# Optimization experiments

Measured on AMD Instinct MI355X. Metric: run time of the kernel, lower is better.

Reference implementation:

```python
import jax, jax.numpy as jnp
import numpy as np
import math

V, E, H, L, S_MAX = 50257, 1024, 16, 4, 1024
D = E // H
F = 4 * E
B, S = 2, 1024


def _ln(x, w, b, eps=1e-5):
    mu = jnp.mean(x, axis=-1, keepdims=True)
    var = jnp.var(x, axis=-1, keepdims=True)
    return (x - mu) * jax.lax.rsqrt(var + eps) * w + b


def setup_inputs() -> dict:
    key = jax.random.key(0)
    ks = jax.random.split(key, 16)
    std = 0.02
    def nrm(k, shape):
        return jax.random.normal(k, shape, dtype=jnp.float32) * std
    inp = {
        'idx': jax.random.randint(ks[0], (B, S), 0, V),
        'tok_emb': nrm(ks[1], (V, E)),
        'pos_emb': jnp.zeros((S_MAX, E), jnp.float32),
        # per-layer stacked params; Linear weights stored [in, out]
        'ln1_w': jnp.ones((L, E), jnp.float32), 'ln1_b': jnp.zeros((L, E), jnp.float32),
        'Wq': nrm(ks[2], (L, E, E)), 'bq': jnp.zeros((L, E), jnp.float32),
        'Wk': nrm(ks[3], (L, E, E)), 'bk': jnp.zeros((L, E), jnp.float32),
        'Wv': nrm(ks[4], (L, E, E)), 'bv': jnp.zeros((L, E), jnp.float32),
        'Wo': nrm(ks[5], (L, E, E)), 'bo': jnp.zeros((L, E), jnp.float32),
        'ln2_w': jnp.ones((L, E), jnp.float32), 'ln2_b': jnp.zeros((L, E), jnp.float32),
        'W1': nrm(ks[6], (L, E, F)), 'b1': jnp.zeros((L, F), jnp.float32),
        'W2': nrm(ks[7], (L, F, E)), 'b2': jnp.zeros((L, E), jnp.float32),
        'lnf_w': jnp.ones((E,), jnp.float32), 'lnf_b': jnp.zeros((E,), jnp.float32),
        'head_W': nrm(ks[8], (V, E)),  # torch Linear weight [out, in], no bias
    }
    return inp


def _gpt(idx, tok_emb, pos_emb, ln1_w, ln1_b, Wq, bq, Wk, bk, Wv, bv, Wo, bo,
         ln2_w, ln2_b, W1, b1, W2, b2, lnf_w, lnf_b, head_W):
    b, s = idx.shape
    x = tok_emb[idx] + pos_emb[None, :s, :]  # [B,S,E]
    causal = jnp.tril(jnp.ones((s, s), bool))
    scale = 1.0 / math.sqrt(D)
    for l in range(L):
        h = _ln(x, ln1_w[l], ln1_b[l])
        q = (h @ Wq[l] + bq[l]).reshape(b, s, H, D).transpose(0, 2, 1, 3)
        k = (h @ Wk[l] + bk[l]).reshape(b, s, H, D).transpose(0, 2, 1, 3)
        v = (h @ Wv[l] + bv[l]).reshape(b, s, H, D).transpose(0, 2, 1, 3)
        scores = jnp.einsum('bhsd,bhtd->bhst', q, k) * scale
        scores = jnp.where(causal, scores, -jnp.inf)
        attn = jax.nn.softmax(scores, axis=-1)
        y = jnp.einsum('bhst,bhtd->bhsd', attn, v)
        y = y.transpose(0, 2, 1, 3).reshape(b, s, E)
        x = x + y @ Wo[l] + bo[l]
        h2 = _ln(x, ln2_w[l], ln2_b[l])
        x = x + jax.nn.gelu(h2 @ W1[l] + b1[l], approximate=False) @ W2[l] + b2[l]
    x = _ln(x, lnf_w, lnf_b)
    return x @ head_W.T  # logits [B,S,V]


def reference(idx, tok_emb, pos_emb, ln1_w, ln1_b, Wq, bq, Wk, bk, Wv, bv, Wo, bo,
              ln2_w, ln2_b, W1, b1, W2, b2, lnf_w, lnf_b, head_W):
    return _gpt(idx, tok_emb, pos_emb, ln1_w, ln1_b, Wq, bq, Wk, bk, Wv, bv, Wo, bo,
                ln2_w, ln2_b, W1, b1, W2, b2, lnf_w, lnf_b, head_W)
```

## Files before the change

kernel.cpp:

```cpp
#include <hip/hip_runtime.h>
#include <hip/hip_bf16.h>
#include <math.h>

#define E_DIM 1024
#define H_NUM 16
#define D_DIM 64
#define F_DIM 4096
#define L_NUM 4
#define B_NUM 2
#define S_LEN 1024
#define V_DIM 50257
#define M_TOK 2048

typedef __attribute__((ext_vector_type(8))) short s8v;
typedef __attribute__((ext_vector_type(4))) float f4v;

static __device__ __forceinline__ float bf2f(unsigned short u) {
    union { unsigned int i; float f; } c; c.i = ((unsigned int)u) << 16; return c.f;
}
static __device__ __forceinline__ unsigned short f2bf(float f) {
    union { float f; unsigned int i; } c; c.f = f;
    unsigned int r = c.i + 0x7FFFu + ((c.i >> 16) & 1u);
    return (unsigned short)(r >> 16);
}

static __device__ __forceinline__ void gload16(const ushort* g, ushort* l) {
    __builtin_amdgcn_global_load_lds(
        (const __attribute__((address_space(1))) unsigned int*)g,
        (__attribute__((address_space(3))) unsigned int*)l, 16, 0, 0);
}

__global__ void embed_kernel(const int* __restrict__ idx,
                             const float* __restrict__ tok,
                             const float* __restrict__ pos,
                             float* __restrict__ x) {
    int row = blockIdx.x;
    int s = row & (S_LEN - 1);
    int t = idx[row];
    const float* te = tok + (size_t)t * E_DIM;
    const float* pe = pos + (size_t)s * E_DIM;
    float* xr = x + (size_t)row * E_DIM;
    int c = threadIdx.x * 4;
    float4 a = *(const float4*)(te + c);
    float4 p = *(const float4*)(pe + c);
    float4 o; o.x = a.x + p.x; o.y = a.y + p.y; o.z = a.z + p.z; o.w = a.w + p.w;
    *(float4*)(xr + c) = o;
}

__global__ void ln_kernel(const float* __restrict__ x,
                          const float* __restrict__ w,
                          const float* __restrict__ b,
                          ushort* __restrict__ out) {
    int row = blockIdx.x;
    const float* xr = x + (size_t)row * E_DIM;
    int tid = threadIdx.x;
    float4 v = *(const float4*)(xr + tid * 4);
    float s  = v.x + v.y + v.z + v.w;
    float s2 = v.x*v.x + v.y*v.y + v.z*v.z + v.w*v.w;
    #pragma unroll
    for (int m = 32; m >= 1; m >>= 1) {
        s  += __shfl_xor(s,  m, 64);
        s2 += __shfl_xor(s2, m, 64);
    }
    __shared__ float red[8];
    int wid = tid >> 6;
    if ((tid & 63) == 0) { red[wid] = s; red[wid + 4] = s2; }
    __syncthreads();
    s  = red[0] + red[1] + red[2] + red[3];
    s2 = red[4] + red[5] + red[6] + red[7];
    float mu  = s * (1.0f / E_DIM);
    float var = s2 * (1.0f / E_DIM) - mu * mu;
    float rs  = rsqrtf(var + 1e-5f);
    float4 wv = *(const float4*)(w + tid * 4);
    float4 bv = *(const float4*)(b + tid * 4);
    ushort4 o;
    o.x = f2bf((v.x - mu) * rs * wv.x + bv.x);
    o.y = f2bf((v.y - mu) * rs * wv.y + bv.y);
    o.z = f2bf((v.z - mu) * rs * wv.z + bv.z);
    o.w = f2bf((v.w - mu) * rs * wv.w + bv.w);
    *(ushort4*)(out + (size_t)row * E_DIM + tid * 4) = o;
}

static __device__ __forceinline__ void tconv_body(
    const float* __restrict__ in, ushort* __restrict__ out, int K, int N, int bx, int by)
{
    __shared__ ushort t[64][72];
    int n0 = bx * 64, k0 = by * 64;
    int tid = threadIdx.x;
    int r = tid >> 4, c = (tid & 15) * 4;
    #pragma unroll
    for (int it = 0; it < 4; ++it) {
        int kl = it * 16 + r;
        float4 v = *(const float4*)(in + (size_t)(k0 + kl) * N + n0 + c);
        t[kl][c]   = f2bf(v.x); t[kl][c+1] = f2bf(v.y);
        t[kl][c+2] = f2bf(v.z); t[kl][c+3] = f2bf(v.w);
    }
    __syncthreads();
    int nl = tid >> 2, k8 = (tid & 3) * 16;
    s8v o0, o1;
    #pragma unroll
    for (int j = 0; j < 8; ++j) o0[j] = (short)t[k8 + j][nl];
    #pragma unroll
    for (int j = 0; j < 8; ++j) o1[j] = (short)t[k8 + 8 + j][nl];
    *(s8v*)(out + (size_t)(n0 + nl) * K + k0 + k8)     = o0;
    *(s8v*)(out + (size_t)(n0 + nl) * K + k0 + k8 + 8) = o1;
}

__global__ __launch_bounds__(256) void tconv_kernel(const float* __restrict__ in,
                                                    ushort* __restrict__ out, int K, int N) {
    tconv_body(in, out, K, N, blockIdx.x, blockIdx.y);
}

__global__ __launch_bounds__(256) void tconv_qkvo_all(
    const float* __restrict__ Wq, const float* __restrict__ Wk,
    const float* __restrict__ Wv, const float* __restrict__ Wo,
    ushort* __restrict__ out)
{
    int z = blockIdx.z, l = z >> 2, w = z & 3;
    const float* in = (w == 0 ? Wq : w == 1 ? Wk : w == 2 ? Wv : Wo)
                      + (size_t)l * E_DIM * E_DIM;
    tconv_body(in, out + (size_t)z * E_DIM * E_DIM, E_DIM, E_DIM, blockIdx.x, blockIdx.y);
}

__global__ __launch_bounds__(256) void tconv_w_all(
    const float* __restrict__ W, ushort* __restrict__ out, int K, int N)
{
    int l = blockIdx.z;
    tconv_body(W + (size_t)l * K * N, out + (size_t)l * K * N, K, N, blockIdx.x, blockIdx.y);
}

__global__ void conv_kernel(const float* __restrict__ in, ushort* __restrict__ out, int n) {
    int i = (blockIdx.x * 256 + threadIdx.x) * 8;
    if (i + 8 <= n) {
        float4 a = *(const float4*)(in + i);
        float4 b = *(const float4*)(in + i + 4);
        s8v o;
        o[0]=(short)f2bf(a.x); o[1]=(short)f2bf(a.y); o[2]=(short)f2bf(a.z); o[3]=(short)f2bf(a.w);
        o[4]=(short)f2bf(b.x); o[5]=(short)f2bf(b.y); o[6]=(short)f2bf(b.z); o[7]=(short)f2bf(b.w);
        *(s8v*)(out + i) = o;
    }
}

#define KSTR 72
#define VSTR 144
__global__ __launch_bounds__(512, 4) void attn_mfma_kernel(
    const ushort* __restrict__ qg, const ushort* __restrict__ kg,
    const ushort* __restrict__ vg, ushort* __restrict__ yg)
{
    __shared__ ushort smem[27648];
    ushort (*Ks)[KSTR] = (ushort(*)[KSTR])smem;
    ushort (*Vt)[VSTR] = (ushort(*)[VSTR])(smem + 128 * KSTR);
    ushort (*Ps)[16][KSTR] = (ushort(*)[16][KSTR])(smem + 128 * KSTR + 64 * VSTR);
    float* mb = (float*)smem;

    int tid = threadIdx.x;
    int wid = tid >> 6, lane = tid & 63;
    int c = lane & 15, g = lane >> 4;
    int grp = wid >> 2, ws = wid & 3;

    int head = blockIdx.x & 31;
    int qt = 15 - (blockIdx.x >> 5);
    int b = head >> 4, h = head & 15;
    int qw = qt * 64 + ws * 16;
    size_t base = (size_t)b * S_LEN * E_DIM + (size_t)(h * D_DIM);

    s8v qf[2];
    #pragma unroll
    for (int ks = 0; ks < 2; ++ks)
        qf[ks] = *(const s8v*)(qg + base + (size_t)(qw + c) * E_DIM + ks * 32 + g * 8);

    f4v o[4];
    #pragma unroll
    for (int dt = 0; dt < 4; ++dt) o[dt] = (f4v){0.f, 0.f, 0.f, 0.f};
    float m[4], lsum[4];
    #pragma unroll
    for (int j = 0; j < 4; ++j) { m[j] = -1e30f; lsum[j] = 0.f; }

    int nr = (qt >> 1) + 1;
    for (int r = 0; r < nr; ++r) {
        int t0 = r * 128;
        #pragma unroll
        for (int it = 0; it < 2; ++it) {
            int ch = tid + it * 512;
            int tr = ch >> 3, dc = (ch & 7) << 3;
            s8v kv = *(const s8v*)(kg + base + (size_t)(t0 + tr) * E_DIM + dc);
            *(s8v*)(&Ks[tr][dc]) = kv;
            s8v vv = *(const s8v*)(vg + base + (size_t)(t0 + tr) * E_DIM + dc);
            int tsw = tr ^ dc;
            #pragma unroll
            for (int j = 0; j < 8; ++j)
                Vt[dc + j][tsw] = (ushort)vv[j];
        }
        __syncthreads();

        int myt = r * 2 + grp;
        if (myt <= qt) {
            int toff = grp * 64;
            f4v s4[4];
            #pragma unroll
            for (int tj = 0; tj < 4; ++tj) {
                s4[tj] = (f4v){0.f, 0.f, 0.f, 0.f};
                #pragma unroll
                for (int ks = 0; ks < 2; ++ks) {
                    s8v kf = *(const s8v*)(&Ks[toff + tj * 16 + c][ks * 32 + g * 8]);
                    s4[tj] = __builtin_amdgcn_mfma_f32_16x16x32_bf16(qf[ks], kf, s4[tj], 0, 0, 0);
                }
            }

            bool diag = (myt == qt);
            float sc[4][4], pm[4];
            #pragma unroll
            for (int j = 0; j < 4; ++j) pm[j] = -1e30f;
            #pragma unroll
            for (int tj = 0; tj < 4; ++tj)
                #pragma unroll
                for (int j = 0; j < 4; ++j) {
                    float val = s4[tj][j] * 0.125f;
                    if (diag) {
                        int t_loc = tj * 16 + c;
                        int q_loc = ws * 16 + 4 * g + j;
                        if (t_loc > q_loc) val = -1e30f;
                    }
                    sc[tj][j] = val;
                    pm[j] = fmaxf(pm[j], val);
                }
            #pragma unroll
            for (int msk = 1; msk <= 8; msk <<= 1)
                #pragma unroll
                for (int j = 0; j < 4; ++j)
                    pm[j] = fmaxf(pm[j], __shfl_xor(pm[j], msk, 64));
            float rs[4], corr[4];
            #pragma unroll
            for (int j = 0; j < 4; ++j) {
                float nm = fmaxf(m[j], pm[j]);
                corr[j] = __expf(m[j] - nm);
                m[j] = nm;
                rs[j] = 0.f;
            }
            #pragma unroll
            for (int tj = 0; tj < 4; ++tj)
                #pragma unroll
                for (int j = 0; j < 4; ++j) {
                    float p = __expf(sc[tj][j] - m[j]);
                    rs[j] += p;
                    Ps[wid][4 * g + j][(tj * 16 + c) ^ (g << 3)] = f2bf(p);
                }
            #pragma unroll
            for (int msk = 1; msk <= 8; msk <<= 1)
                #pragma unroll
                for (int j = 0; j < 4; ++j)
                    rs[j] += __shfl_xor(rs[j], msk, 64);
            #pragma unroll
            for (int j = 0; j < 4; ++j) lsum[j] = lsum[j] * corr[j] + rs[j];
            #pragma unroll
            for (int dt = 0; dt < 4; ++dt)
                #pragma unroll
                for (int j = 0; j < 4; ++j) o[dt][j] *= corr[j];

            #pragma unroll
            for (int ks = 0; ks < 2; ++ks) {
                int blk = g + 4 * ks;
                int pblk = blk ^ (c >> 2);
                s8v pa = *(const s8v*)(&Ps[wid][c][pblk << 3]);
                int tb = grp * 8 + blk;
                #pragma unroll
                for (int dt = 0; dt < 4; ++dt) {
                    int d = dt * 16 + c;
                    int vblk = tb ^ ((d >> 3) & 7);
                    s8v vb = *(const s8v*)(&Vt[d][vblk << 3]);
                    o[dt] = __builtin_amdgcn_mfma_f32_16x16x32_bf16(pa, vb, o[dt], 0, 0, 0);
                }
            }
        }
        __syncthreads();
    }

    if (grp == 1) {
        float* dst = mb + (ws * 64 + lane) * 25;
        #pragma unroll
        for (int j = 0; j < 4; ++j) { dst[j] = m[j]; dst[4 + j] = lsum[j]; }
        #pragma unroll
        for (int dt = 0; dt < 4; ++dt)
            #pragma unroll
            for (int j = 0; j < 4; ++j) dst[8 + dt * 4 + j] = o[dt][j];
    }
    __syncthreads();
    if (grp == 0) {
        const float* src = mb + (ws * 64 + lane) * 25;
        float sA[4], sB[4];
        #pragma unroll
        for (int j = 0; j < 4; ++j) {
            float mB = src[j], lB = src[4 + j];
            float mN = fmaxf(m[j], mB);
            sA[j] = __expf(m[j] - mN);
            sB[j] = __expf(mB - mN);
            lsum[j] = lsum[j] * sA[j] + lB * sB[j];
        }
        float inv[4];
        #pragma unroll
        for (int j = 0; j < 4; ++j) inv[j] = 1.f / lsum[j];
        #pragma unroll
        for (int dt = 0; dt < 4; ++dt)
            #pragma unroll
            for (int j = 0; j < 4; ++j) {
                float ov = o[dt][j] * sA[j] + src[8 + dt * 4 + j] * sB[j];
                yg[base + (size_t)(qw + 4 * g + j) * E_DIM + dt * 16 + c] = f2bf(ov * inv[j]);
            }
    }
}

template<int EPI>
static __device__ __forceinline__ void gemm_bb_body(
    const ushort* __restrict__ A, const ushort* __restrict__ B,
    const float* __restrict__ bias, const float* __restrict__ res,
    float* __restrict__ outF, ushort* __restrict__ outB,
    int Ndim, int Kdim, int m0, int n0, int nRows)
{
    __shared__ ushort As[128 * 64];
    __shared__ ushort Bs[128 * 64];
    int tid = threadIdx.x;
    int wid = tid >> 6, lane = tid & 63;
    int wr = wid >> 1, wc = wid & 1;
    int fr = lane & 15, fq = lane >> 4;
    int lr = lane >> 3, ls = lane & 7;

    f4v acc[4][4];
    #pragma unroll
    for (int mi = 0; mi < 4; ++mi)
        #pragma unroll
        for (int ni = 0; ni < 4; ++ni)
            acc[mi][ni] = (f4v){0.f, 0.f, 0.f, 0.f};

    for (int k0 = 0; k0 < Kdim; k0 += 64) {
        #pragma unroll
        for (int it = 0; it < 4; ++it) {
            int r = wid * 32 + it * 8 + lr;
            int ss = ls ^ (r & 7);
            gload16(A + (size_t)(m0 + r) * Kdim + k0 + ss * 8,
                    As + r * 64 - lr * 64 - ls * 8);
        }
        #pragma unroll
        for (int it = 0; it < 4; ++it) {
            int r = wid * 32 + it * 8 + lr;
            int ss = ls ^ (r & 7);
            int br = n0 + r; if (br >= nRows) br = nRows - 1;
            gload16(B + (size_t)br * Kdim + k0 + ss * 8,
                    Bs + r * 64 - lr * 64 - ls * 8);
        }
        __syncthreads();
        #pragma unroll
        for (int ks = 0; ks < 2; ++ks) {
            s8v af[4], bfv[4];
            #pragma unroll
            for (int mi = 0; mi < 4; ++mi) {
                int Ra = wr * 64 + mi * 16 + fr;
                int Sa = (ks * 4 + fq) ^ (fr & 7);
                af[mi] = *(const s8v*)(As + Ra * 64 + Sa * 8);
            }
            #pragma unroll
            for (int ni = 0; ni < 4; ++ni) {
                int Rb = wc * 64 + ni * 16 + fr;
                int Sb = (ks * 4 + fq) ^ (fr & 7);
                bfv[ni] = *(const s8v*)(Bs + Rb * 64 + Sb * 8);
            }
            #pragma unroll
            for (int mi = 0; mi < 4; ++mi)
                #pragma unroll
                for (int ni = 0; ni < 4; ++ni)
                    acc[mi][ni] = __builtin_amdgcn_mfma_f32_16x16x32_bf16(
                        af[mi], bfv[ni], acc[mi][ni], 0, 0, 0);
        }
        __syncthreads();
    }

    #pragma unroll
    for (int mi = 0; mi < 4; ++mi) {
        int row = m0 + wr * 64 + mi * 16 + fq * 4;
        #pragma unroll
        for (int ni = 0; ni < 4; ++ni) {
            int col = n0 + wc * 64 + ni * 16 + fr;
            float bv = 0.f;
            if (EPI == 0 || EPI == 1 || EPI == 2) bv = bias[col];
            #pragma unroll
            for (int j = 0; j < 4; ++j) {
                float val = acc[mi][ni][j] + bv;
                size_t off = (size_t)(row + j) * Ndim + col;
                if (EPI == 0) {
                    outB[off] = f2bf(val);
                } else if (EPI == 1) {
                    outF[off] = res[off] + val;
                } else if (EPI == 2) {
                    val = 0.5f * val * (1.f + erff(val * 0.70710678118654752f));
                    outB[off] = f2bf(val);
                } else {
                    if (col < Ndim) outF[off] = val;
                }
            }
        }
    }
}

template<int EPI>
__global__ __launch_bounds__(256) void gemm_bb_kernel(
    const ushort* __restrict__ A, const ushort* __restrict__ B,
    const float* __restrict__ bias, const float* __restrict__ res,
    float* __restrict__ outF, ushort* __restrict__ outB,
    int Ndim, int Kdim, int nRows)
{
    int x = blockIdx.x & 7, i = blockIdx.x >> 3;
    int mb = x * 2 + (i & 1), nb = i >> 1;
    gemm_bb_body<EPI>(A, B, bias, res, outF, outB, Ndim, Kdim, mb * 128, nb * 128, nRows);
}

__global__ __launch_bounds__(256) void gemm_qkv_bb_kernel(
    const ushort* __restrict__ A,
    const ushort* __restrict__ Bq, const ushort* __restrict__ Bk, const ushort* __restrict__ Bv,
    const float* __restrict__ bq, const float* __restrict__ bk, const float* __restrict__ bv,
    ushort* __restrict__ oq, ushort* __restrict__ ok, ushort* __restrict__ ov)
{
    int x = blockIdx.x & 7, i = blockIdx.x >> 3;
    int sel = i >> 4, j = i & 15;
    int mb = x * 2 + (j & 1), nb = j >> 1;
    const ushort* B   = (sel == 0) ? Bq : (sel == 1) ? Bk : Bv;
    const float* bias = (sel == 0) ? bq : (sel == 1) ? bk : bv;
    ushort* o         = (sel == 0) ? oq : (sel == 1) ? ok : ov;
    gemm_bb_body<0>(A, B, bias, nullptr, nullptr, o, E_DIM, E_DIM, mb * 128, nb * 128, E_DIM);
}

template<int EPI>
static __device__ __forceinline__ void gemm64_body(
    const ushort* __restrict__ A, const ushort* __restrict__ B,
    const float* __restrict__ bias, const float* __restrict__ res,
    float* __restrict__ outF, ushort* __restrict__ outB,
    int Ndim, int Kdim, int m0, int n0)
{
    __shared__ ushort As[64 * 64];
    __shared__ ushort Bs[128 * 64];
    int tid = threadIdx.x;
    int wid = tid >> 6, lane = tid & 63;
    int fr = lane & 15, fq = lane >> 4;
    int lr = lane >> 3, ls = lane & 7;

    f4v acc[4][2];
    #pragma unroll
    for (int mi = 0; mi < 4; ++mi)
        #pragma unroll
        for (int ni = 0; ni < 2; ++ni)
            acc[mi][ni] = (f4v){0.f, 0.f, 0.f, 0.f};

    for (int k0 = 0; k0 < Kdim; k0 += 64) {
        #pragma unroll
        for (int it = 0; it < 2; ++it) {
            int r = wid * 16 + it * 8 + lr;
            int ss = ls ^ (r & 7);
            gload16(A + (size_t)(m0 + r) * Kdim + k0 + ss * 8,
                    As + r * 64 - lr * 64 - ls * 8);
        }
        #pragma unroll
        for (int it = 0; it < 4; ++it) {
            int r = wid * 32 + it * 8 + lr;
            int ss = ls ^ (r & 7);
            gload16(B + (size_t)(n0 + r) * Kdim + k0 + ss * 8,
                    Bs + r * 64 - lr * 64 - ls * 8);
        }
        __syncthreads();
        #pragma unroll
        for (int ks = 0; ks < 2; ++ks) {
            s8v af[4], bfv[2];
            #pragma unroll
            for (int mi = 0; mi < 4; ++mi) {
                int Ra = mi * 16 + fr;
                int Sa = (ks * 4 + fq) ^ (fr & 7);
                af[mi] = *(const s8v*)(As + Ra * 64 + Sa * 8);
            }
            #pragma unroll
            for (int ni = 0; ni < 2; ++ni) {
                int Rb = wid * 32 + ni * 16 + fr;
                int Sb = (ks * 4 + fq) ^ (fr & 7);
                bfv[ni] = *(const s8v*)(Bs + Rb * 64 + Sb * 8);
            }
            #pragma unroll
            for (int mi = 0; mi < 4; ++mi)
                #pragma unroll
                for (int ni = 0; ni < 2; ++ni)
                    acc[mi][ni] = __builtin_amdgcn_mfma_f32_16x16x32_bf16(
                        af[mi], bfv[ni], acc[mi][ni], 0, 0, 0);
        }
        __syncthreads();
    }

    #pragma unroll
    for (int mi = 0; mi < 4; ++mi) {
        int row = m0 + mi * 16 + fq * 4;
        #pragma unroll
        for (int ni = 0; ni < 2; ++ni) {
            int col = n0 + wid * 32 + ni * 16 + fr;
            float bv = bias[col];
            #pragma unroll
            for (int j = 0; j < 4; ++j) {
                float val = acc[mi][ni][j] + bv;
                size_t off = (size_t)(row + j) * Ndim + col;
                if (EPI == 0) {
                    outB[off] = f2bf(val);
                } else {
                    outF[off] = res[off] + val;
                }
            }
        }
    }
}

template<int EPI>
__global__ __launch_bounds__(256) void gemm64_kernel(
    const ushort* __restrict__ A, const ushort* __restrict__ B,
    const float* __restrict__ bias, const float* __restrict__ res,
    float* __restrict__ outF, ushort* __restrict__ outB,
    int Ndim, int Kdim)
{
    int x = blockIdx.x & 7, i = blockIdx.x >> 3;
    int mb = x * 4 + (i & 3), nb = i >> 2;
    gemm64_body<EPI>(A, B, bias, res, outF, outB, Ndim, Kdim, mb * 64, nb * 128);
}

__global__ __launch_bounds__(256) void gemm64_qkv_kernel(
    const ushort* __restrict__ A, const ushort* __restrict__ Wall,
    const float* __restrict__ bq, const float* __restrict__ bk, const float* __restrict__ bv,
    ushort* __restrict__ oq, ushort* __restrict__ ok, ushort* __restrict__ ov)
{
    int x = blockIdx.x & 7, i = blockIdx.x >> 3;
    int sel = i >> 5, j = i & 31;
    int mb = x * 4 + (j & 3), nb = j >> 2;
    const ushort* B   = Wall + (size_t)sel * E_DIM * E_DIM;
    const float* bias = (sel == 0) ? bq : (sel == 1) ? bk : bv;
    ushort* o         = (sel == 0) ? oq : (sel == 1) ? ok : ov;
    gemm64_body<0>(A, B, bias, nullptr, nullptr, o, E_DIM, E_DIM, mb * 64, nb * 128);
}

extern "C" void kernel_launch(void* const* d_in, const int* in_sizes, int n_in,
                              void* d_out, int out_size, void* d_ws, size_t ws_size,
                              hipStream_t stream) {
    (void)in_sizes; (void)n_in; (void)out_size;
    const int*   idx  = (const int*)d_in[0];
    const float* tok  = (const float*)d_in[1];
    const float* pos  = (const float*)d_in[2];
    const float* ln1w = (const float*)d_in[3];
    const float* ln1b = (const float*)d_in[4];
    const float* Wq   = (const float*)d_in[5];
    const float* bq   = (const float*)d_in[6];
    const float* Wk   = (const float*)d_in[7];
    const float* bk   = (const float*)d_in[8];
    const float* Wv   = (const float*)d_in[9];
    const float* bv   = (const float*)d_in[10];
    const float* Wo   = (const float*)d_in[11];
    const float* bo   = (const float*)d_in[12];
    const float* ln2w = (const float*)d_in[13];
    const float* ln2b = (const float*)d_in[14];
    const float* W1   = (const float*)d_in[15];
    const float* b1   = (const float*)d_in[16];
    const float* W2   = (const float*)d_in[17];
    const float* b2   = (const float*)d_in[18];
    const float* lnfw = (const float*)d_in[19];
    const float* lnfb = (const float*)d_in[20];
    const float* headW= (const float*)d_in[21];
    float* out = (float*)d_out;

    char* ws = (char*)d_ws;
    float*  x  = (float*)(ws);
    ushort* h  = (ushort*)(ws + 8u  * 1024 * 1024);
    ushort* qb = (ushort*)(ws + 12u * 1024 * 1024);
    ushort* kb = (ushort*)(ws + 16u * 1024 * 1024);
    ushort* vb = (ushort*)(ws + 20u * 1024 * 1024);
    ushort* yb = (ushort*)(ws + 24u * 1024 * 1024);
    ushort* ub = (ushort*)(ws + 28u * 1024 * 1024);
    ushort* wqb = (ushort*)(ws + 44u * 1024 * 1024);
    ushort* wkb = (ushort*)(ws + 46u * 1024 * 1024);
    ushort* wvb = (ushort*)(ws + 48u * 1024 * 1024);
    ushort* wob = (ushort*)(ws + 50u * 1024 * 1024);
    ushort* w1b = (ushort*)(ws + 52u * 1024 * 1024);
    ushort* w2b = (ushort*)(ws + 60u * 1024 * 1024);
    ushort* hdbM = (ushort*)(ws + 68u * 1024 * 1024);
    ushort* wall  = (ushort*)(ws + 44u  * 1024 * 1024);
    ushort* w1all = (ushort*)(ws + 76u  * 1024 * 1024);
    ushort* w2all = (ushort*)(ws + 108u * 1024 * 1024);
    ushort* hdbH  = (ushort*)(ws + 140u * 1024 * 1024);

    size_t headB = (size_t)V_DIM * E_DIM * 2;
    bool huge = ws_size >= 140ull * 1024 * 1024 + headB;
    bool big  = ws_size >= 68ull * 1024 * 1024 + headB;
    bool mid  = ws_size >= 68ull * 1024 * 1024;

    dim3 blk(256);
    dim3 blkA(512);
    embed_kernel<<<dim3(M_TOK), blk, 0, stream>>>(idx, tok, pos, x);

    if (huge) {
        tconv_qkvo_all<<<dim3(16, 16, 16), blk, 0, stream>>>(Wq, Wk, Wv, Wo, wall);
        tconv_w_all<<<dim3(64, 16, 4), blk, 0, stream>>>(W1, w1all, E_DIM, F_DIM);
        tconv_w_all<<<dim3(16, 64, 4), blk, 0, stream>>>(W2, w2all, F_DIM, E_DIM);
        int n = V_DIM * E_DIM;
        conv_kernel<<<dim3((n / 8 + 255) / 256), blk, 0, stream>>>(headW, hdbH, n);

        for (int l = 0; l < L_NUM; ++l) {
            const ushort* wl  = wall  + (size_t)(l * 4) * E_DIM * E_DIM;
            const ushort* wol = wall  + (size_t)(l * 4 + 3) * E_DIM * E_DIM;
            const ushort* w1l = w1all + (size_t)l * E_DIM * F_DIM;
            const ushort* w2l = w2all + (size_t)l * F_DIM * E_DIM;

            ln_kernel<<<dim3(M_TOK), blk, 0, stream>>>(x, ln1w + l * E_DIM, ln1b + l * E_DIM, h);
            gemm64_qkv_kernel<<<dim3(768), blk, 0, stream>>>(h, wl,
                bq + l*E_DIM, bk + l*E_DIM, bv + l*E_DIM, qb, kb, vb);
            attn_mfma_kernel<<<dim3(512), blkA, 0, stream>>>(qb, kb, vb, yb);
            gemm64_kernel<1><<<dim3(256), blk, 0, stream>>>(yb, wol, bo + l*E_DIM, x, x, nullptr, E_DIM, E_DIM);
            ln_kernel<<<dim3(M_TOK), blk, 0, stream>>>(x, ln2w + l * E_DIM, ln2b + l * E_DIM, h);
            gemm_bb_kernel<2><<<dim3(512), blk, 0, stream>>>(h, w1l, b1 + l*F_DIM, nullptr, nullptr, ub, F_DIM, E_DIM, F_DIM);
            gemm64_kernel<1><<<dim3(256), blk, 0, stream>>>(ub, w2l, b2 + l*E_DIM, x, x, nullptr, E_DIM, F_DIM);
        }
        ln_kernel<<<dim3(M_TOK), blk, 0, stream>>>(x, lnfw, lnfb, h);
        gemm_bb_kernel<3><<<dim3(6288), blk, 0, stream>>>(h, hdbH, nullptr, nullptr, out, nullptr, V_DIM, E_DIM, V_DIM);
        return;
    }

    if (big) {
        int n = V_DIM * E_DIM;
        conv_kernel<<<dim3((n / 8 + 255) / 256), blk, 0, stream>>>(headW, hdbM, n);
    }

    for (int l = 0; l < L_NUM; ++l) {
        const float* wq = Wq + (size_t)l * E_DIM * E_DIM;
        const float* wk = Wk + (size_t)l * E_DIM * E_DIM;
        const float* wv = Wv + (size_t)l * E_DIM * E_DIM;
        const float* wo = Wo + (size_t)l * E_DIM * E_DIM;
        const float* w1 = W1 + (size_t)l * E_DIM * F_DIM;
        const float* w2 = W2 + (size_t)l * F_DIM * E_DIM;

        ln_kernel<<<dim3(M_TOK), blk, 0, stream>>>(x, ln1w + l * E_DIM, ln1b + l * E_DIM, h);
        if (mid) {
            tconv_kernel<<<dim3(16, 16), blk, 0, stream>>>(wq, wqb, E_DIM, E_DIM);
            tconv_kernel<<<dim3(16, 16), blk, 0, stream>>>(wk, wkb, E_DIM, E_DIM);
            tconv_kernel<<<dim3(16, 16), blk, 0, stream>>>(wv, wvb, E_DIM, E_DIM);
            tconv_kernel<<<dim3(16, 16), blk, 0, stream>>>(wo, wob, E_DIM, E_DIM);
            tconv_kernel<<<dim3(64, 16), blk, 0, stream>>>(w1, w1b, E_DIM, F_DIM);
            tconv_kernel<<<dim3(16, 64), blk, 0, stream>>>(w2, w2b, F_DIM, E_DIM);

            gemm_qkv_bb_kernel<<<dim3(384), blk, 0, stream>>>(h, wqb, wkb, wvb,
                bq + l*E_DIM, bk + l*E_DIM, bv + l*E_DIM, qb, kb, vb);
            attn_mfma_kernel<<<dim3(512), blkA, 0, stream>>>(qb, kb, vb, yb);
            gemm_bb_kernel<1><<<dim3(128), blk, 0, stream>>>(yb, wob, bo + l*E_DIM, x, x, nullptr, E_DIM, E_DIM, E_DIM);
            ln_kernel<<<dim3(M_TOK), blk, 0, stream>>>(x, ln2w + l * E_DIM, ln2b + l * E_DIM, h);
            gemm_bb_kernel<2><<<dim3(512), blk, 0, stream>>>(h, w1b, b1 + l*F_DIM, nullptr, nullptr, ub, F_DIM, E_DIM, F_DIM);
            gemm_bb_kernel<1><<<dim3(128), blk, 0, stream>>>(ub, w2b, b2 + l*E_DIM, x, x, nullptr, E_DIM, F_DIM, E_DIM);
        }
    }

    ln_kernel<<<dim3(M_TOK), blk, 0, stream>>>(x, lnfw, lnfb, h);
    if (big) {
        gemm_bb_kernel<3><<<dim3(6288), blk, 0, stream>>>(h, hdbM, nullptr, nullptr, out, nullptr, V_DIM, E_DIM, V_DIM);
    }
}
```

Measured before the change: 1.173 ms.

## Add 256x256-tile double-buffered MFMA GEMM for LM head projection

Adds a dedicated kernel for the vocabulary projection that uses 256x256 output tiles, 512 threads, swizzled LDS and double-buffered K tiles with global-to-LDS loads. It replaces the smaller-tile generic GEMM for the head in both code paths. The larger tiles raise operand reuse and cut redundant loads of h and head weights. The cost is higher register and LDS pressure, plus wasted work in the padded last N tile.

```diff
diff --git a/kernel.cpp b/kernel.cpp
--- a/kernel.cpp
+++ b/kernel.cpp
@@ -534,6 +534,96 @@
     const float* bias = (sel == 0) ? bq : (sel == 1) ? bk : bv;
     ushort* o         = (sel == 0) ? oq : (sel == 1) ? ok : ov;
     gemm64_body<0>(A, B, bias, nullptr, nullptr, o, E_DIM, E_DIM, mb * 64, nb * 128);
+}
+
+__global__ __launch_bounds__(512, 2) void gemm256_head_kernel(
+    const ushort* __restrict__ A, const ushort* __restrict__ B,
+    float* __restrict__ outF, int Ndim, int Kdim, int nRows)
+{
+    __shared__ ushort As[2][256 * 32];
+    __shared__ ushort Bs[2][256 * 32];
+    int tid = threadIdx.x;
+    int wid = tid >> 6, lane = tid & 63;
+    int wr = wid >> 2, wc = wid & 3;
+    int fr = lane & 15, fq = lane >> 4;
+
+    int mb = blockIdx.x & 7, nb = blockIdx.x >> 3;
+    int m0 = mb * 256, n0 = nb * 256;
+
+    int srow = (lane >> 2);
+    int lslot = lane & 3;
+
+    f4v acc[8][4];
+    #pragma unroll
+    for (int mi = 0; mi < 8; ++mi)
+        #pragma unroll
+        for (int ni = 0; ni < 4; ++ni)
+            acc[mi][ni] = (f4v){0.f, 0.f, 0.f, 0.f};
+
+    #pragma unroll
+    for (int rr = 0; rr < 2; ++rr) {
+        int row = wid * 16 + rr * 128 + srow;
+        int sg = lslot ^ (row & 3) ^ ((row >> 2) & 3);
+        gload16(A + (size_t)(m0 + row) * Kdim + sg * 8,
+                &As[0][(wid * 16 + rr * 128) * 32]);
+        int br = n0 + row; if (br >= nRows) br = nRows - 1;
+        gload16(B + (size_t)br * Kdim + sg * 8,
+                &Bs[0][(wid * 16 + rr * 128) * 32]);
+    }
+    __syncthreads();
+
+    int nt = Kdim >> 5;
+    int cur = 0;
+    for (int t = 0; t < nt; ++t) {
+        if (t + 1 < nt) {
+            int k0 = (t + 1) << 5;
+            #pragma unroll
+            for (int rr = 0; rr < 2; ++rr) {
+                int row = wid * 16 + rr * 128 + srow;
+                int sg = lslot ^ (row & 3) ^ ((row >> 2) & 3);
+                gload16(A + (size_t)(m0 + row) * Kdim + k0 + sg * 8,
+                        &As[cur ^ 1][(wid * 16 + rr * 128) * 32]);
+                int br = n0 + row; if (br >= nRows) br = nRows - 1;
+                gload16(B + (size_t)br * Kdim + k0 + sg * 8,
+                        &Bs[cur ^ 1][(wid * 16 + rr * 128) * 32]);
+            }
+        }
+        s8v bfv[4];
+        #pragma unroll
+        for (int ni = 0; ni < 4; ++ni) {
+            int Rb = wc * 64 + ni * 16 + fr;
+            int sl = fq ^ (Rb & 3) ^ ((Rb >> 2) & 3);
+            bfv[ni] = *(const s8v*)(&Bs[cur][Rb * 32 + sl * 8]);
+        }
+        __builtin_amdgcn_s_setprio(1);
+        #pragma unroll
+        for (int mi = 0; mi < 8; ++mi) {
+            int Ra = wr * 128 + mi * 16 + fr;
+            int sl = fq ^ (Ra & 3) ^ ((Ra >> 2) & 3);
+            s8v af = *(const s8v*)(&As[cur][Ra * 32 + sl * 8]);
+            #pragma unroll
+            for (int ni = 0; ni < 4; ++ni)
+                acc[mi][ni] = __builtin_amdgcn_mfma_f32_16x16x32_bf16(
+                    af, bfv[ni], acc[mi][ni], 0, 0, 0);
+        }
+        __builtin_amdgcn_s_setprio(0);
+        __syncthreads();
+        cur ^= 1;
+    }
+
+    #pragma unroll
+    for (int mi = 0; mi < 8; ++mi) {
+        int row = m0 + wr * 128 + mi * 16 + fq * 4;
+        #pragma unroll
+        for (int ni = 0; ni < 4; ++ni) {
+            int col = n0 + wc * 64 + ni * 16 + fr;
+            if (col < Ndim) {
+                #pragma unroll
+                for (int j = 0; j < 4; ++j)
+                    outF[(size_t)(row + j) * Ndim + col] = acc[mi][ni][j];
+            }
+        }
+    }
 }
 
 extern "C" void kernel_launch(void* const* d_in, const int* in_sizes, int n_in,
@@ -616,7 +706,7 @@
             gemm64_kernel<1><<<dim3(256), blk, 0, stream>>>(ub, w2l, b2 + l*E_DIM, x, x, nullptr, E_DIM, F_DIM);
         }
         ln_kernel<<<dim3(M_TOK), blk, 0, stream>>>(x, lnfw, lnfb, h);
-        gemm_bb_kernel<3><<<dim3(6288), blk, 0, stream>>>(h, hdbH, nullptr, nullptr, out, nullptr, V_DIM, E_DIM, V_DIM);
+        gemm256_head_kernel<<<dim3(1576), blkA, 0, stream>>>(h, hdbH, out, V_DIM, E_DIM, V_DIM);
         return;
     }
 
@@ -654,6 +744,6 @@
 
     ln_kernel<<<dim3(M_TOK), blk, 0, stream>>>(x, lnfw, lnfb, h);
     if (big) {
-        gemm_bb_kernel<3><<<dim3(6288), blk, 0, stream>>>(h, hdbM, nullptr, nullptr, out, nullptr, V_DIM, E_DIM, V_DIM);
-    }
-}
+        gemm256_head_kernel<<<dim3(1576), blkA, 0, stream>>>(h, hdbM, out, V_DIM, E_DIM, V_DIM);
+    }
+}
```

Result: slower. 1.294 ms (+10.3%).
